# Optimization experiments

Measured on AMD Instinct MI355X. Metric: run time of the kernel, lower is better.

## Reference

```python
import jax, jax.numpy as jnp
import numpy as np

N = 8_388_608
C = 3  # 3 sentiment classes; |argmax - y| == 2 <=> class-0/class-2 confusion


def setup_inputs() -> dict:
    key = jax.random.key(0)
    k1, k2 = jax.random.split(key)
    logits = jax.random.normal(k1, (N, C), dtype=jnp.float32)
    # original module expects log-softmax outputs
    pre = jax.nn.log_softmax(logits, axis=-1)
    y_true = jax.random.randint(k2, (N,), 0, C, dtype=jnp.int64)
    weight = jnp.float32(2.0)
    return {"pre": pre, "y_true": y_true, "weight": weight}


def reference(pre, y_true, weight):
    # gather log-prob of true class: pre[i, y_true[i]]
    picked = jnp.take_along_axis(pre, y_true[:, None], axis=1)[:, 0]  # [N]
    pred = jnp.argmax(pre, axis=-1)                                   # [N]
    # penalize opposite-polarity mistakes (|pred - y| == 2)
    penal = jnp.abs(pred - y_true) == 2                               # [N] bool
    w = jnp.where(penal, weight, jnp.float32(1.0))                    # [N]
    return -jnp.sum(w * picked) / jnp.float32(pre.shape[0])
```

## Files before the change

kernel.cpp:

```cpp
#include <hip/hip_runtime.h>


#define N_ROWS   8388608
#define BLOCK    256
#define GRID     1024
#define WPB      (BLOCK / 64)
#define NWAVES   (GRID * WPB)
#define CHUNK    256
#define NITER    (N_ROWS / (NWAVES * CHUNK))
#define ROWS_PW  (CHUNK * NITER)

__global__ __launch_bounds__(BLOCK) void nll_fused_kernel(
        const float* __restrict__ pre,
        const int*   __restrict__ y_true,
        const float* __restrict__ wptr,
        float*       __restrict__ out) {
    __shared__ float tile[WPB][2][768];
    __shared__ float red[WPB];

    const float wgt  = wptr[0];
    const int   t    = threadIdx.x;
    const int   lane = t & 63;
    const int   wv   = t >> 6;
    const int   W    = (int)blockIdx.x * WPB + wv;

    const float4* __restrict__ pre4 = (const float4*)pre;

    const int fbW = W * (ROWS_PW * 3 / 4);
    const int ybW = W * ROWS_PW;

    float4 v[2][3];
    int    yv[2][4];

    #pragma unroll
    for (int p = 0; p < 2; ++p) {
        const int fb = fbW + p * 192;
        const int yb = ybW + p * 256;
        v[p][0] = pre4[fb +       lane];
        v[p][1] = pre4[fb +  64 + lane];
        v[p][2] = pre4[fb + 128 + lane];
        yv[p][0] = y_true[yb +       lane];
        yv[p][1] = y_true[yb +  64 + lane];
        yv[p][2] = y_true[yb + 128 + lane];
        yv[p][3] = y_true[yb + 192 + lane];
    }

    float acc = 0.0f;
    #pragma unroll
    for (int k = 0; k < NITER; ++k) {
        const int b = k & 1;
        float*  slice = tile[wv][b];
        float4* s4    = (float4*)slice;

        s4[       lane] = v[b][0];
        s4[ 64 +  lane] = v[b][1];
        s4[128 +  lane] = v[b][2];

        const int y0 = yv[b][0], y1 = yv[b][1], y2 = yv[b][2], y3 = yv[b][3];

        if (k + 2 < NITER) {
            const int fb = fbW + (k + 2) * 192;
            const int yb = ybW + (k + 2) * 256;
            v[b][0] = pre4[fb +       lane];
            v[b][1] = pre4[fb +  64 + lane];
            v[b][2] = pre4[fb + 128 + lane];
            yv[b][0] = y_true[yb +       lane];
            yv[b][1] = y_true[yb +  64 + lane];
            yv[b][2] = y_true[yb + 128 + lane];
            yv[b][3] = y_true[yb + 192 + lane];
        }

        asm volatile("s_waitcnt lgkmcnt(0)" ::: "memory");

        const int yls[4] = {y0, y1, y2, y3};
        #pragma unroll
        for (int m = 0; m < 4; ++m) {
            const int   w0 = 3 * lane + 192 * m;
            const float p0 = slice[w0 + 0];
            const float p1 = slice[w0 + 1];
            const float p2 = slice[w0 + 2];
            const int   tt = yls[m];
            const float picked = (tt == 0) ? p0 : ((tt == 1) ? p1 : p2);
            int   prd = 0;
            float mx  = p0;
            if (p1 > mx) { mx = p1; prd = 1; }
            if (p2 > mx) { prd = 2; }
            const bool penal = (prd - tt == 2) || (tt - prd == 2);
            acc += (penal ? wgt : 1.0f) * picked;
        }
    }

    #pragma unroll
    for (int off = 32; off > 0; off >>= 1)
        acc += __shfl_down(acc, off, 64);

    if (lane == 0) red[wv] = acc;
    __syncthreads();

    if (t == 0) {
        const float s = red[0] + red[1] + red[2] + red[3];
        atomicAdd(out, s * (-1.0f / (float)N_ROWS));
    }
}

extern "C" void kernel_launch(void* const* d_in, const int* in_sizes, int n_in,
                              void* d_out, int out_size, void* d_ws, size_t ws_size,
                              hipStream_t stream) {
    const float* pre  = (const float*)d_in[0];
    const int*   y    = (const int*)d_in[1];
    const float* wptr = (const float*)d_in[2];
    float* out = (float*)d_out;

    nll_fused_kernel<<<GRID, BLOCK, 0, stream>>>(pre, y, wptr, out);
}
```

Before: 175.5 us.

## Use nontemporal loads, triple-buffer prefetch registers, and two-pass deterministic reduction

New measurement: 159.5 us (median of 2 runs). 9.1% less time.

```diff
diff --git a/kernel.cpp b/kernel.cpp
--- a/kernel.cpp
+++ b/kernel.cpp
@@ -1,5 +1,7 @@
 #include <hip/hip_runtime.h>
 
+
+typedef float v4f __attribute__((ext_vector_type(4)));
 
 #define N_ROWS   8388608
 #define BLOCK    256
@@ -10,11 +12,11 @@
 #define NITER    (N_ROWS / (NWAVES * CHUNK))
 #define ROWS_PW  (CHUNK * NITER)
 
-__global__ __launch_bounds__(BLOCK) void nll_fused_kernel(
+__global__ __launch_bounds__(BLOCK) void nll_main(
         const float* __restrict__ pre,
         const int*   __restrict__ y_true,
         const float* __restrict__ wptr,
-        float*       __restrict__ out) {
+        float*       __restrict__ partial) {
     __shared__ float tile[WPB][2][768];
     __shared__ float red[WPB];
 
@@ -24,62 +26,59 @@
     const int   wv   = t >> 6;
     const int   W    = (int)blockIdx.x * WPB + wv;
 
-    const float4* __restrict__ pre4 = (const float4*)pre;
-
+    const v4f* __restrict__ pre4 = (const v4f*)pre;
     const int fbW = W * (ROWS_PW * 3 / 4);
     const int ybW = W * ROWS_PW;
 
-    float4 v[2][3];
-    int    yv[2][4];
+    v4f v[3][3];
+    int yv[3][4];
 
     #pragma unroll
     for (int p = 0; p < 2; ++p) {
         const int fb = fbW + p * 192;
         const int yb = ybW + p * 256;
-        v[p][0] = pre4[fb +       lane];
-        v[p][1] = pre4[fb +  64 + lane];
-        v[p][2] = pre4[fb + 128 + lane];
-        yv[p][0] = y_true[yb +       lane];
-        yv[p][1] = y_true[yb +  64 + lane];
-        yv[p][2] = y_true[yb + 128 + lane];
-        yv[p][3] = y_true[yb + 192 + lane];
+        v[p][0] = __builtin_nontemporal_load(pre4 + fb +       lane);
+        v[p][1] = __builtin_nontemporal_load(pre4 + fb +  64 + lane);
+        v[p][2] = __builtin_nontemporal_load(pre4 + fb + 128 + lane);
+        yv[p][0] = __builtin_nontemporal_load(y_true + yb +       lane);
+        yv[p][1] = __builtin_nontemporal_load(y_true + yb +  64 + lane);
+        yv[p][2] = __builtin_nontemporal_load(y_true + yb + 128 + lane);
+        yv[p][3] = __builtin_nontemporal_load(y_true + yb + 192 + lane);
     }
 
     float acc = 0.0f;
     #pragma unroll
     for (int k = 0; k < NITER; ++k) {
-        const int b = k & 1;
-        float*  slice = tile[wv][b];
-        float4* s4    = (float4*)slice;
+        const int b  = k % 3;
+        const int nb = (k + 2) % 3;
 
+        if (k + 2 < NITER) {
+            const int fb = fbW + (k + 2) * 192;
+            const int yb = ybW + (k + 2) * 256;
+            v[nb][0] = __builtin_nontemporal_load(pre4 + fb +       lane);
+            v[nb][1] = __builtin_nontemporal_load(pre4 + fb +  64 + lane);
+            v[nb][2] = __builtin_nontemporal_load(pre4 + fb + 128 + lane);
+            yv[nb][0] = __builtin_nontemporal_load(y_true + yb +       lane);
+            yv[nb][1] = __builtin_nontemporal_load(y_true + yb +  64 + lane);
+            yv[nb][2] = __builtin_nontemporal_load(y_true + yb + 128 + lane);
+            yv[nb][3] = __builtin_nontemporal_load(y_true + yb + 192 + lane);
+        }
+
+        float* slice = tile[wv][k & 1];
+        v4f*   s4    = (v4f*)slice;
         s4[       lane] = v[b][0];
         s4[ 64 +  lane] = v[b][1];
         s4[128 +  lane] = v[b][2];
 
-        const int y0 = yv[b][0], y1 = yv[b][1], y2 = yv[b][2], y3 = yv[b][3];
-
-        if (k + 2 < NITER) {
-            const int fb = fbW + (k + 2) * 192;
-            const int yb = ybW + (k + 2) * 256;
-            v[b][0] = pre4[fb +       lane];
-            v[b][1] = pre4[fb +  64 + lane];
-            v[b][2] = pre4[fb + 128 + lane];
-            yv[b][0] = y_true[yb +       lane];
-            yv[b][1] = y_true[yb +  64 + lane];
-            yv[b][2] = y_true[yb + 128 + lane];
-            yv[b][3] = y_true[yb + 192 + lane];
-        }
-
         asm volatile("s_waitcnt lgkmcnt(0)" ::: "memory");
 
-        const int yls[4] = {y0, y1, y2, y3};
         #pragma unroll
         for (int m = 0; m < 4; ++m) {
             const int   w0 = 3 * lane + 192 * m;
             const float p0 = slice[w0 + 0];
             const float p1 = slice[w0 + 1];
             const float p2 = slice[w0 + 2];
-            const int   tt = yls[m];
+            const int   tt = yv[b][m];
             const float picked = (tt == 0) ? p0 : ((tt == 1) ? p1 : p2);
             int   prd = 0;
             float mx  = p0;
@@ -97,10 +96,24 @@
     if (lane == 0) red[wv] = acc;
     __syncthreads();
 
-    if (t == 0) {
-        const float s = red[0] + red[1] + red[2] + red[3];
-        atomicAdd(out, s * (-1.0f / (float)N_ROWS));
-    }
+    if (t == 0)
+        partial[blockIdx.x] = red[0] + red[1] + red[2] + red[3];
+}
+
+__global__ __launch_bounds__(256) void nll_reduce(
+        const float* __restrict__ partial,
+        float*       __restrict__ out) {
+    const float4 p = ((const float4*)partial)[threadIdx.x];
+    float s = p.x + p.y + p.z + p.w;
+    #pragma unroll
+    for (int off = 32; off > 0; off >>= 1)
+        s += __shfl_down(s, off, 64);
+
+    __shared__ float r[4];
+    if ((threadIdx.x & 63) == 0) r[threadIdx.x >> 6] = s;
+    __syncthreads();
+    if (threadIdx.x == 0)
+        out[0] = (r[0] + r[1] + r[2] + r[3]) * (-1.0f / (float)N_ROWS);
 }
 
 extern "C" void kernel_launch(void* const* d_in, const int* in_sizes, int n_in,
@@ -109,7 +122,9 @@
     const float* pre  = (const float*)d_in[0];
     const int*   y    = (const int*)d_in[1];
     const float* wptr = (const float*)d_in[2];
+    float* ws  = (float*)d_ws;
     float* out = (float*)d_out;
 
-    nll_fused_kernel<<<GRID, BLOCK, 0, stream>>>(pre, y, wptr, out);
+    nll_main<<<GRID, BLOCK, 0, stream>>>(pre, y, wptr, ws);
+    nll_reduce<<<1, 256, 0, stream>>>(ws, out);
 }
```
